# Kernel optimization log

Hardware: AMD Instinct MI355X
Metric: run time of the kernel (lower is better)

## Reference

```python
import jax, jax.numpy as jnp
import numpy as np

B, DIN, DOUT, NC = 8192, 4096, 4096, 64


def setup_inputs() -> dict:
    key = jax.random.key(0)
    k1, k2, k3, k4, k5 = jax.random.split(key, 5)
    x = jax.random.normal(k1, (B, DIN), dtype=jnp.float32)
    cluster = jax.random.uniform(k2, (B, NC), dtype=jnp.float32)
    weight = jax.random.uniform(k3, (DIN, DOUT), dtype=jnp.float32,
                                minval=-0.25, maxval=0.25)
    # torch init is ones; perturb slightly so the modulation is non-trivial
    style_L = 1.0 + 0.1 * jax.random.normal(k4, (NC, DIN), dtype=jnp.float32)
    style_R = 1.0 + 0.1 * jax.random.normal(k5, (NC, DOUT), dtype=jnp.float32)
    return {"x": x, "cluster": cluster, "weight": weight,
            "style_L": style_L, "style_R": style_R}


def reference(x, cluster, weight, style_L, style_R):
    # tmp_L: (B, din), tmp_R: (B, dout)
    tmp_L = cluster @ style_L
    tmp_R = cluster @ style_R
    # Algebraically identical to (weight * outer(tmp_L, tmp_R)) applied per
    # sample: out[b,o] = sum_i x[b,i]*tmpL[b,i]*W[i,o]*tmpR[b,o].
    # Factorized form avoids the (B, din, dout) intermediate.
    return ((x * tmp_L) @ weight) * tmp_R
```

## Files before the change

### kernel.cpp

```cpp
#include <hip/hip_runtime.h>
#include <cstdint>

#define BB   8192
#define DIN  4096
#define DOUT 4096
#define NCL  64

typedef __bf16 bf16;
typedef __attribute__((ext_vector_type(8))) __bf16 bf16x8;
typedef __attribute__((ext_vector_type(4))) float   f32x4;

#define GAS(p) (reinterpret_cast<uint32_t __attribute__((address_space(1)))*>(reinterpret_cast<uintptr_t>(p)))
#define LAS(p) (reinterpret_cast<uint32_t __attribute__((address_space(3)))*>(reinterpret_cast<uintptr_t>(p)))

#define WAITV(n)  asm volatile("s_waitcnt vmcnt(" #n ")" ::: "memory")
#define WAITL()   asm volatile("s_waitcnt lgkmcnt(0)" ::: "memory")
#define BARR()    __builtin_amdgcn_s_barrier()
#define SCHED0()  __builtin_amdgcn_sched_barrier(0)
#define MFMA(a, b, c) __builtin_amdgcn_mfma_f32_16x16x32_bf16((a), (b), (c), 0, 0, 0)

__global__ __launch_bounds__(256) void prologue_kernel(
    const float* __restrict__ x, const float* __restrict__ cl,
    const float* __restrict__ sL, bf16* __restrict__ Ap,
    bf16* __restrict__ clb)
{
    __shared__ uint4 lds_u4[2048];
    char* lds = (char*)lds_u4;
    const int t    = threadIdx.x;
    const int lane = t & 63;
    const int w    = t >> 6;
    const int wm   = w >> 1, wn = w & 1;
    const int r0   = blockIdx.x * 128;
    const int c0   = blockIdx.y * 128;

    #pragma unroll
    for (int i = 0; i < 4; i++) {
        int tk  = t + i * 256;
        int row = tk >> 3, ch = tk & 7;
        const float* src = cl + (size_t)(r0 + row) * NCL + ch * 8;
        float4 v0 = *(const float4*)src;
        float4 v1 = *(const float4*)(src + 4);
        bf16x8 pk;
        pk[0]=(bf16)v0.x; pk[1]=(bf16)v0.y; pk[2]=(bf16)v0.z; pk[3]=(bf16)v0.w;
        pk[4]=(bf16)v1.x; pk[5]=(bf16)v1.y; pk[6]=(bf16)v1.z; pk[7]=(bf16)v1.w;
        *(bf16x8*)(lds + row * 128 + ((ch ^ (row & 7)) << 4)) = pk;
        if (blockIdx.y == 0)
            *(bf16x8*)(clb + (size_t)(r0 + row) * NCL + ch * 8) = pk;
    }
    #pragma unroll
    for (int i = 0; i < 4; i++) {
        int tk = t + i * 256;
        int n  = tk & 127, c = tk >> 7;
        bf16x8 pl;
        #pragma unroll
        for (int j = 0; j < 8; j++)
            pl[j] = (bf16)sL[(size_t)(c * 8 + j) * DIN + c0 + n];
        *(bf16x8*)(lds + 16384 + n * 128 + ((c ^ (n & 7)) << 4)) = pl;
    }
    __syncthreads();

    f32x4 accL[4][4] = {};
    #pragma unroll
    for (int s = 0; s < 2; s++) {
        bf16x8 a[4], bl[4];
        #pragma unroll
        for (int m = 0; m < 4; m++) {
            int row = wm * 64 + m * 16 + (lane & 15);
            int ch  = s * 4 + (lane >> 4);
            a[m] = *(bf16x8*)(lds + row * 128 + ((ch ^ (row & 7)) << 4));
        }
        #pragma unroll
        for (int n = 0; n < 4; n++) {
            int row = wn * 64 + n * 16 + (lane & 15);
            int ch  = s * 4 + (lane >> 4);
            bl[n] = *(bf16x8*)(lds + 16384 + row * 128 + ((ch ^ (row & 7)) << 4));
        }
        #pragma unroll
        for (int m = 0; m < 4; m++)
            #pragma unroll
            for (int n = 0; n < 4; n++)
                accL[m][n] = MFMA(a[m], bl[n], accL[m][n]);
    }

    #pragma unroll
    for (int m = 0; m < 4; m++) {
        int rbase = r0 + wm * 64 + m * 16 + ((lane >> 4) << 2);
        #pragma unroll
        for (int n = 0; n < 4; n++) {
            int col = c0 + wn * 64 + n * 16 + (lane & 15);
            #pragma unroll
            for (int j = 0; j < 4; j++) {
                size_t idx = (size_t)(rbase + j) * DIN + col;
                Ap[idx] = (bf16)(x[idx] * accL[m][n][j]);
            }
        }
    }
}

__global__ __launch_bounds__(256) void transpose_kernel(
    const float* __restrict__ W, bf16* __restrict__ Wt)
{
    const int t  = threadIdx.x;
    const int n  = blockIdx.x * 256 + t;
    const int k0 = blockIdx.y * 32;
    bf16x8 v[4];
    #pragma unroll
    for (int q = 0; q < 4; q++)
        #pragma unroll
        for (int j = 0; j < 8; j++)
            v[q][j] = (bf16)W[(size_t)(k0 + q * 8 + j) * DOUT + n];
    bf16* dst = Wt + (size_t)n * DIN + k0;
    #pragma unroll
    for (int q = 0; q < 4; q++)
        *(bf16x8*)(dst + q * 8) = v[q];
}

__global__ __launch_bounds__(256) void srt_kernel(
    const float* __restrict__ sR, bf16* __restrict__ srt)
{
    const int o = blockIdx.x * 256 + threadIdx.x;
    bf16x8 v[8];
    #pragma unroll
    for (int q = 0; q < 8; q++)
        #pragma unroll
        for (int j = 0; j < 8; j++)
            v[q][j] = (bf16)sR[(size_t)(q * 8 + j) * DOUT + o];
    bf16* dst = srt + (size_t)o * 64;
    #pragma unroll
    for (int q = 0; q < 8; q++)
        *(bf16x8*)(dst + q * 8) = v[q];
}

template<int CUR>
__device__ __forceinline__ void tile_step(char* lds, int tid,
    const bf16* pA1, const bf16* pA2, const bf16* pA3, const bf16* pA4,
    const bf16* pB1, const bf16* pB2, const bf16* pB3, const bf16* pB4,
    int kA1, int kA2, int aoff0, int aoff1, int boff0, int boff1,
    bf16x8 a[4][2], bf16x8 b[4][2], f32x4 acc[8][4])
{
    constexpr int CB = CUR * 65536;
    constexpr int OB = (CUR ^ 1) * 65536;

    #pragma unroll
    for (int mq = 0; mq < 4; ++mq) {
        a[mq][0] = *(const bf16x8*)(lds + CB + mq * 2048 + aoff0);
        a[mq][1] = *(const bf16x8*)(lds + CB + mq * 2048 + aoff1);
    }
    #pragma unroll
    for (int nb = 0; nb < 4; ++nb) {
        b[nb][0] = *(const bf16x8*)(lds + CB + nb * 2048 + boff0);
        b[nb][1] = *(const bf16x8*)(lds + CB + nb * 2048 + boff1);
    }
    __builtin_amdgcn_global_load_lds(GAS(pA3 + kA1), LAS(lds + OB + 16384 + tid * 16), 16, 0, 0);
    __builtin_amdgcn_global_load_lds(GAS(pA4 + kA1), LAS(lds + OB + 24576 + tid * 16), 16, 0, 0);
    BARR();
    WAITL(); SCHED0();
    __builtin_amdgcn_s_setprio(1);
    #pragma unroll
    for (int k = 0; k < 2; ++k)
        #pragma unroll
        for (int mq = 0; mq < 4; ++mq)
            #pragma unroll
            for (int nq = 0; nq < 2; ++nq)
                acc[mq][nq] = MFMA(a[mq][k], b[nq][k], acc[mq][nq]);
    __builtin_amdgcn_s_setprio(0);
    BARR();

    __builtin_amdgcn_global_load_lds(GAS(pB1 + kA2), LAS(lds + CB + 32768 + tid * 16), 16, 0, 0);
    __builtin_amdgcn_global_load_lds(GAS(pB2 + kA2), LAS(lds + CB + 40960 + tid * 16), 16, 0, 0);
    BARR();
    __builtin_amdgcn_s_setprio(1);
    #pragma unroll
    for (int k = 0; k < 2; ++k)
        #pragma unroll
        for (int mq = 0; mq < 4; ++mq)
            #pragma unroll
            for (int nq = 0; nq < 2; ++nq)
                acc[mq][2 + nq] = MFMA(a[mq][k], b[2 + nq][k], acc[mq][2 + nq]);
    __builtin_amdgcn_s_setprio(0);
    BARR();

    #pragma unroll
    for (int mq = 0; mq < 4; ++mq) {
        a[mq][0] = *(const bf16x8*)(lds + CB + 8192 + mq * 2048 + aoff0);
        a[mq][1] = *(const bf16x8*)(lds + CB + 8192 + mq * 2048 + aoff1);
    }
    __builtin_amdgcn_global_load_lds(GAS(pB3 + kA2), LAS(lds + CB + 49152 + tid * 16), 16, 0, 0);
    __builtin_amdgcn_global_load_lds(GAS(pB4 + kA2), LAS(lds + CB + 57344 + tid * 16), 16, 0, 0);
    BARR();
    WAITL(); SCHED0();
    __builtin_amdgcn_s_setprio(1);
    #pragma unroll
    for (int k = 0; k < 2; ++k)
        #pragma unroll
        for (int mq = 0; mq < 4; ++mq)
            #pragma unroll
            for (int nq = 0; nq < 2; ++nq)
                acc[4 + mq][2 + nq] = MFMA(a[mq][k], b[2 + nq][k], acc[4 + mq][2 + nq]);
    __builtin_amdgcn_s_setprio(0);
    BARR();

    __builtin_amdgcn_global_load_lds(GAS(pA1 + kA2), LAS(lds + CB + tid * 16), 16, 0, 0);
    __builtin_amdgcn_global_load_lds(GAS(pA2 + kA2), LAS(lds + CB + 8192 + tid * 16), 16, 0, 0);
    BARR();
    __builtin_amdgcn_s_setprio(1);
    #pragma unroll
    for (int k = 0; k < 2; ++k)
        #pragma unroll
        for (int mq = 0; mq < 4; ++mq)
            #pragma unroll
            for (int nq = 0; nq < 2; ++nq)
                acc[4 + mq][nq] = MFMA(a[mq][k], b[nq][k], acc[4 + mq][nq]);
    __builtin_amdgcn_s_setprio(0);
    WAITV(6);
    BARR();
}

__global__ __launch_bounds__(512, 2) void gemm_kernel(
    const bf16* __restrict__ Ap, const bf16* __restrict__ Wt,
    const bf16* __restrict__ clb, const bf16* __restrict__ srt,
    float* __restrict__ out)
{
    __shared__ uint4 smem[8192];
    char* lds = (char*)smem;
    const int tid  = threadIdx.x;
    const int lane = tid & 63;
    const int w    = tid >> 6;
    const int wm   = w >> 2;
    const int wn   = w & 3;
    const int L = lane & 15, H = lane >> 4;

    const int bid = blockIdx.x;
    const int xc  = bid & 7, ii = bid >> 3;
    const int mt  = xc * 4 + (ii >> 4);
    const int nt  = ii & 15;
    const size_t brow = (size_t)mt * 256;
    const size_t bcol = (size_t)nt * 256;

    const int r1  = tid >> 3;
    const int gch = (tid & 7) ^ (r1 & 7);
    const bf16* pA1 = Ap + (brow + r1) * (size_t)DIN + gch * 8;
    const bf16* pA2 = pA1 + (size_t)64  * DIN;
    const bf16* pA3 = pA1 + (size_t)128 * DIN;
    const bf16* pA4 = pA1 + (size_t)192 * DIN;
    const bf16* pB1 = Wt + (bcol + r1) * (size_t)DIN + gch * 8;
    const bf16* pB2 = pB1 + (size_t)64  * DIN;
    const bf16* pB3 = pB1 + (size_t)128 * DIN;
    const bf16* pB4 = pB1 + (size_t)192 * DIN;

    const int swz0 = (H ^ (L & 7)) << 4;
    const int swz1 = ((4 + H) ^ (L & 7)) << 4;
    const int aoff0 = wm * 16384 + L * 128 + swz0;
    const int aoff1 = wm * 16384 + L * 128 + swz1;
    const int boff0 = 32768 + (wn >> 1) * 16384 + (wn & 1) * 8192 + L * 128 + swz0;
    const int boff1 = 32768 + (wn >> 1) * 16384 + (wn & 1) * 8192 + L * 128 + swz1;

    bf16x8 a[4][2], b[4][2];
    f32x4 acc[8][4] = {};

    __builtin_amdgcn_global_load_lds(GAS(pA1), LAS(lds + tid * 16), 16, 0, 0);
    __builtin_amdgcn_global_load_lds(GAS(pA2), LAS(lds + 8192 + tid * 16), 16, 0, 0);
    __builtin_amdgcn_global_load_lds(GAS(pA3), LAS(lds + 16384 + tid * 16), 16, 0, 0);
    __builtin_amdgcn_global_load_lds(GAS(pA4), LAS(lds + 24576 + tid * 16), 16, 0, 0);
    __builtin_amdgcn_global_load_lds(GAS(pB1), LAS(lds + 32768 + tid * 16), 16, 0, 0);
    __builtin_amdgcn_global_load_lds(GAS(pB2), LAS(lds + 40960 + tid * 16), 16, 0, 0);
    __builtin_amdgcn_global_load_lds(GAS(pB3), LAS(lds + 49152 + tid * 16), 16, 0, 0);
    __builtin_amdgcn_global_load_lds(GAS(pB4), LAS(lds + 57344 + tid * 16), 16, 0, 0);
    __builtin_amdgcn_global_load_lds(GAS(pB1 + 64), LAS(lds + 65536 + 32768 + tid * 16), 16, 0, 0);
    __builtin_amdgcn_global_load_lds(GAS(pB2 + 64), LAS(lds + 65536 + 40960 + tid * 16), 16, 0, 0);
    __builtin_amdgcn_global_load_lds(GAS(pB3 + 64), LAS(lds + 65536 + 49152 + tid * 16), 16, 0, 0);
    __builtin_amdgcn_global_load_lds(GAS(pB4 + 64), LAS(lds + 65536 + 57344 + tid * 16), 16, 0, 0);
    __builtin_amdgcn_global_load_lds(GAS(pA1 + 64), LAS(lds + 65536 + tid * 16), 16, 0, 0);
    __builtin_amdgcn_global_load_lds(GAS(pA2 + 64), LAS(lds + 65536 + 8192 + tid * 16), 16, 0, 0);
    WAITV(6);
    BARR();

    #pragma unroll 1
    for (int t = 0; t < 64; t += 2) {
        tile_step<0>(lds, tid, pA1, pA2, pA3, pA4, pB1, pB2, pB3, pB4,
                     ((t + 1) & 63) * 64, ((t + 2) & 63) * 64,
                     aoff0, aoff1, boff0, boff1, a, b, acc);
        tile_step<1>(lds, tid, pA1, pA2, pA3, pA4, pB1, pB2, pB3, pB4,
                     ((t + 2) & 63) * 64, ((t + 3) & 63) * 64,
                     aoff0, aoff1, boff0, boff1, a, b, acc);
    }

    WAITV(0);
    const bf16* pC = clb + (brow + r1) * 64 + gch * 8;
    const bf16* pR = srt + (bcol + r1) * 64 + gch * 8;
    __builtin_amdgcn_global_load_lds(GAS(pC),         LAS(lds + tid * 16), 16, 0, 0);
    __builtin_amdgcn_global_load_lds(GAS(pC + 4096),  LAS(lds + 8192 + tid * 16), 16, 0, 0);
    __builtin_amdgcn_global_load_lds(GAS(pC + 8192),  LAS(lds + 16384 + tid * 16), 16, 0, 0);
    __builtin_amdgcn_global_load_lds(GAS(pC + 12288), LAS(lds + 24576 + tid * 16), 16, 0, 0);
    __builtin_amdgcn_global_load_lds(GAS(pR),         LAS(lds + 32768 + tid * 16), 16, 0, 0);
    __builtin_amdgcn_global_load_lds(GAS(pR + 4096),  LAS(lds + 40960 + tid * 16), 16, 0, 0);
    __builtin_amdgcn_global_load_lds(GAS(pR + 8192),  LAS(lds + 49152 + tid * 16), 16, 0, 0);
    __builtin_amdgcn_global_load_lds(GAS(pR + 12288), LAS(lds + 57344 + tid * 16), 16, 0, 0);
    WAITV(0);
    BARR();

    #pragma unroll
    for (int nb = 0; nb < 4; ++nb) {
        b[nb][0] = *(const bf16x8*)(lds + nb * 2048 + boff0);
        b[nb][1] = *(const bf16x8*)(lds + nb * 2048 + boff1);
    }
    #pragma unroll
    for (int half = 0; half < 2; ++half) {
        #pragma unroll
        for (int mq = 0; mq < 4; ++mq) {
            a[mq][0] = *(const bf16x8*)(lds + half * 8192 + mq * 2048 + aoff0);
            a[mq][1] = *(const bf16x8*)(lds + half * 8192 + mq * 2048 + aoff1);
        }
        WAITL(); SCHED0();
        f32x4 r4[4][4] = {};
        #pragma unroll
        for (int k = 0; k < 2; ++k)
            #pragma unroll
            for (int mq = 0; mq < 4; ++mq)
                #pragma unroll
                for (int nb = 0; nb < 4; ++nb)
                    r4[mq][nb] = MFMA(a[mq][k], b[nb][k], r4[mq][nb]);
        #pragma unroll
        for (int mq = 0; mq < 4; ++mq)
            #pragma unroll
            for (int nb = 0; nb < 4; ++nb)
                acc[half * 4 + mq][nb] *= r4[mq][nb];
    }

    #pragma unroll
    for (int m = 0; m < 8; m++) {
        size_t rbase = brow + (size_t)(wm * 128 + m * 16 + (H << 2));
        #pragma unroll
        for (int n = 0; n < 4; n++) {
            size_t col = bcol + (size_t)(wn * 64 + n * 16 + L);
            #pragma unroll
            for (int j = 0; j < 4; j++) {
                size_t idx = (rbase + j) * DOUT + col;
                out[idx] = acc[m][n][j];
            }
        }
    }
}

extern "C" void kernel_launch(void* const* d_in, const int* in_sizes, int n_in,
                              void* d_out, int out_size, void* d_ws, size_t ws_size,
                              hipStream_t stream)
{
    (void)in_sizes; (void)n_in; (void)out_size;
    const float* x  = (const float*)d_in[0];
    const float* cl = (const float*)d_in[1];
    const float* W  = (const float*)d_in[2];
    const float* sL = (const float*)d_in[3];
    const float* sR = (const float*)d_in[4];
    float* out = (float*)d_out;

    const size_t AP_BYTES = (size_t)BB * DIN * sizeof(bf16);
    const size_t WT_BYTES = (size_t)DIN * DOUT * sizeof(bf16);
    const size_t CL_BYTES = (size_t)BB * NCL * sizeof(bf16);
    const size_t SR_BYTES = (size_t)DOUT * NCL * sizeof(bf16);
    if (ws_size < AP_BYTES + WT_BYTES + CL_BYTES + SR_BYTES) return;

    char* ws = (char*)d_ws;
    bf16* Ap  = (bf16*)ws;
    bf16* Wt  = (bf16*)(ws + AP_BYTES);
    bf16* clb = (bf16*)(ws + AP_BYTES + WT_BYTES);
    bf16* srt = (bf16*)(ws + AP_BYTES + WT_BYTES + CL_BYTES);

    prologue_kernel<<<dim3(BB / 128, DIN / 128), 256, 0, stream>>>(x, cl, sL, Ap, clb);
    transpose_kernel<<<dim3(DOUT / 256, DIN / 32), 256, 0, stream>>>(W, Wt);
    srt_kernel<<<dim3(DOUT / 256), 256, 0, stream>>>(sR, srt);
    gemm_kernel<<<dim3((BB / 256) * (DOUT / 256)), 512, 0, stream>>>(Ap, Wt, clb, srt, out);
}
```

Baseline: 330.6 us.

## Switch main GEMM to 32x32x16 MFMA with reworked per-warp tiling and load order

```diff
diff --git a/kernel.cpp b/kernel.cpp
--- a/kernel.cpp
+++ b/kernel.cpp
@@ -7,17 +7,20 @@
 #define NCL  64
 
 typedef __bf16 bf16;
-typedef __attribute__((ext_vector_type(8))) __bf16 bf16x8;
-typedef __attribute__((ext_vector_type(4))) float   f32x4;
+typedef __attribute__((ext_vector_type(8)))  __bf16 bf16x8;
+typedef __attribute__((ext_vector_type(4)))  float  f32x4;
+typedef __attribute__((ext_vector_type(16))) float  f32x16;
 
 #define GAS(p) (reinterpret_cast<uint32_t __attribute__((address_space(1)))*>(reinterpret_cast<uintptr_t>(p)))
 #define LAS(p) (reinterpret_cast<uint32_t __attribute__((address_space(3)))*>(reinterpret_cast<uintptr_t>(p)))
 
 #define WAITV(n)  asm volatile("s_waitcnt vmcnt(" #n ")" ::: "memory")
+#define WAITLN(n) asm volatile("s_waitcnt lgkmcnt(" #n ")" ::: "memory")
 #define WAITL()   asm volatile("s_waitcnt lgkmcnt(0)" ::: "memory")
 #define BARR()    __builtin_amdgcn_s_barrier()
 #define SCHED0()  __builtin_amdgcn_sched_barrier(0)
-#define MFMA(a, b, c) __builtin_amdgcn_mfma_f32_16x16x32_bf16((a), (b), (c), 0, 0, 0)
+#define MFMA16(a, b, c) __builtin_amdgcn_mfma_f32_16x16x32_bf16((a), (b), (c), 0, 0, 0)
+#define MFMA32(a, b, c) __builtin_amdgcn_mfma_f32_32x32x16_bf16((a), (b), (c), 0, 0, 0)
 
 __global__ __launch_bounds__(256) void prologue_kernel(
     const float* __restrict__ x, const float* __restrict__ cl,
@@ -79,7 +82,7 @@
         for (int m = 0; m < 4; m++)
             #pragma unroll
             for (int n = 0; n < 4; n++)
-                accL[m][n] = MFMA(a[m], bl[n], accL[m][n]);
+                accL[m][n] = MFMA16(a[m], bl[n], accL[m][n]);
     }
 
     #pragma unroll
@@ -135,82 +138,79 @@
 __device__ __forceinline__ void tile_step(char* lds, int tid,
     const bf16* pA1, const bf16* pA2, const bf16* pA3, const bf16* pA4,
     const bf16* pB1, const bf16* pB2, const bf16* pB3, const bf16* pB4,
-    int kA1, int kA2, int aoff0, int aoff1, int boff0, int boff1,
-    bf16x8 a[4][2], bf16x8 b[4][2], f32x4 acc[8][4])
+    int kA1, int kA2, int arow, int brow,
+    int ks0, int ks1, int ks2, int ks3,
+    bf16x8 (&a)[2][4], bf16x8 (&b0)[4], bf16x8 (&b1)[4], f32x16 (&acc)[4][2])
 {
     constexpr int CB = CUR * 65536;
     constexpr int OB = (CUR ^ 1) * 65536;
-
-    #pragma unroll
-    for (int mq = 0; mq < 4; ++mq) {
-        a[mq][0] = *(const bf16x8*)(lds + CB + mq * 2048 + aoff0);
-        a[mq][1] = *(const bf16x8*)(lds + CB + mq * 2048 + aoff1);
-    }
-    #pragma unroll
-    for (int nb = 0; nb < 4; ++nb) {
-        b[nb][0] = *(const bf16x8*)(lds + CB + nb * 2048 + boff0);
-        b[nb][1] = *(const bf16x8*)(lds + CB + nb * 2048 + boff1);
-    }
+    const int ks[4] = {ks0, ks1, ks2, ks3};
+
+    #pragma unroll
+    for (int f = 0; f < 2; ++f)
+        #pragma unroll
+        for (int kk = 0; kk < 4; ++kk)
+            a[f][kk] = *(const bf16x8*)(lds + CB + f * 4096 + arow + ks[kk]);
+    #pragma unroll
+    for (int kk = 0; kk < 4; ++kk)
+        b0[kk] = *(const bf16x8*)(lds + CB + 32768 + brow + ks[kk]);
     __builtin_amdgcn_global_load_lds(GAS(pA3 + kA1), LAS(lds + OB + 16384 + tid * 16), 16, 0, 0);
     __builtin_amdgcn_global_load_lds(GAS(pA4 + kA1), LAS(lds + OB + 24576 + tid * 16), 16, 0, 0);
+    WAITLN(8);
     BARR();
     WAITL(); SCHED0();
     __builtin_amdgcn_s_setprio(1);
     #pragma unroll
-    for (int k = 0; k < 2; ++k)
-        #pragma unroll
-        for (int mq = 0; mq < 4; ++mq)
-            #pragma unroll
-            for (int nq = 0; nq < 2; ++nq)
-                acc[mq][nq] = MFMA(a[mq][k], b[nq][k], acc[mq][nq]);
+    for (int kk = 0; kk < 4; ++kk)
+        #pragma unroll
+        for (int f = 0; f < 2; ++f)
+            acc[f][0] = MFMA32(a[f][kk], b0[kk], acc[f][0]);
     __builtin_amdgcn_s_setprio(0);
     BARR();
 
+    #pragma unroll
+    for (int kk = 0; kk < 4; ++kk)
+        b1[kk] = *(const bf16x8*)(lds + CB + 49152 + brow + ks[kk]);
+    __builtin_amdgcn_global_load_lds(GAS(pA1 + kA2), LAS(lds + CB + tid * 16), 16, 0, 0);
+    __builtin_amdgcn_global_load_lds(GAS(pA2 + kA2), LAS(lds + CB + 8192 + tid * 16), 16, 0, 0);
+    BARR();
+    WAITL(); SCHED0();
+    __builtin_amdgcn_s_setprio(1);
+    #pragma unroll
+    for (int kk = 0; kk < 4; ++kk)
+        #pragma unroll
+        for (int f = 0; f < 2; ++f)
+            acc[f][1] = MFMA32(a[f][kk], b1[kk], acc[f][1]);
+    __builtin_amdgcn_s_setprio(0);
+    BARR();
+
+    #pragma unroll
+    for (int f = 0; f < 2; ++f)
+        #pragma unroll
+        for (int kk = 0; kk < 4; ++kk)
+            a[f][kk] = *(const bf16x8*)(lds + CB + 16384 + f * 4096 + arow + ks[kk]);
     __builtin_amdgcn_global_load_lds(GAS(pB1 + kA2), LAS(lds + CB + 32768 + tid * 16), 16, 0, 0);
     __builtin_amdgcn_global_load_lds(GAS(pB2 + kA2), LAS(lds + CB + 40960 + tid * 16), 16, 0, 0);
     BARR();
+    WAITL(); SCHED0();
     __builtin_amdgcn_s_setprio(1);
     #pragma unroll
-    for (int k = 0; k < 2; ++k)
-        #pragma unroll
-        for (int mq = 0; mq < 4; ++mq)
-            #pragma unroll
-            for (int nq = 0; nq < 2; ++nq)
-                acc[mq][2 + nq] = MFMA(a[mq][k], b[2 + nq][k], acc[mq][2 + nq]);
+    for (int kk = 0; kk < 4; ++kk)
+        #pragma unroll
+        for (int f = 0; f < 2; ++f)
+            acc[2 + f][1] = MFMA32(a[f][kk], b1[kk], acc[2 + f][1]);
     __builtin_amdgcn_s_setprio(0);
     BARR();
 
-    #pragma unroll
-    for (int mq = 0; mq < 4; ++mq) {
-        a[mq][0] = *(const bf16x8*)(lds + CB + 8192 + mq * 2048 + aoff0);
-        a[mq][1] = *(const bf16x8*)(lds + CB + 8192 + mq * 2048 + aoff1);
-    }
     __builtin_amdgcn_global_load_lds(GAS(pB3 + kA2), LAS(lds + CB + 49152 + tid * 16), 16, 0, 0);
     __builtin_amdgcn_global_load_lds(GAS(pB4 + kA2), LAS(lds + CB + 57344 + tid * 16), 16, 0, 0);
     BARR();
-    WAITL(); SCHED0();
     __builtin_amdgcn_s_setprio(1);
     #pragma unroll
-    for (int k = 0; k < 2; ++k)
-        #pragma unroll
-        for (int mq = 0; mq < 4; ++mq)
-            #pragma unroll
-            for (int nq = 0; nq < 2; ++nq)
-                acc[4 + mq][2 + nq] = MFMA(a[mq][k], b[2 + nq][k], acc[4 + mq][2 + nq]);
-    __builtin_amdgcn_s_setprio(0);
-    BARR();
-
-    __builtin_amdgcn_global_load_lds(GAS(pA1 + kA2), LAS(lds + CB + tid * 16), 16, 0, 0);
-    __builtin_amdgcn_global_load_lds(GAS(pA2 + kA2), LAS(lds + CB + 8192 + tid * 16), 16, 0, 0);
-    BARR();
-    __builtin_amdgcn_s_setprio(1);
-    #pragma unroll
-    for (int k = 0; k < 2; ++k)
-        #pragma unroll
-        for (int mq = 0; mq < 4; ++mq)
-            #pragma unroll
-            for (int nq = 0; nq < 2; ++nq)
-                acc[4 + mq][nq] = MFMA(a[mq][k], b[nq][k], acc[4 + mq][nq]);
+    for (int kk = 0; kk < 4; ++kk)
+        #pragma unroll
+        for (int f = 0; f < 2; ++f)
+            acc[2 + f][0] = MFMA32(a[f][kk], b0[kk], acc[2 + f][0]);
     __builtin_amdgcn_s_setprio(0);
     WAITV(6);
     BARR();
@@ -228,35 +228,35 @@
     const int w    = tid >> 6;
     const int wm   = w >> 2;
     const int wn   = w & 3;
-    const int L = lane & 15, H = lane >> 4;
+    const int L5 = lane & 31, H1 = lane >> 5;
 
     const int bid = blockIdx.x;
     const int xc  = bid & 7, ii = bid >> 3;
     const int mt  = xc * 4 + (ii >> 4);
     const int nt  = ii & 15;
-    const size_t brow = (size_t)mt * 256;
-    const size_t bcol = (size_t)nt * 256;
+    const size_t brow_g = (size_t)mt * 256;
+    const size_t bcol_g = (size_t)nt * 256;
 
     const int r1  = tid >> 3;
     const int gch = (tid & 7) ^ (r1 & 7);
-    const bf16* pA1 = Ap + (brow + r1) * (size_t)DIN + gch * 8;
+    const bf16* pA1 = Ap + (brow_g + r1) * (size_t)DIN + gch * 8;
     const bf16* pA2 = pA1 + (size_t)64  * DIN;
     const bf16* pA3 = pA1 + (size_t)128 * DIN;
     const bf16* pA4 = pA1 + (size_t)192 * DIN;
-    const bf16* pB1 = Wt + (bcol + r1) * (size_t)DIN + gch * 8;
+    const bf16* pB1 = Wt + (bcol_g + r1) * (size_t)DIN + gch * 8;
     const bf16* pB2 = pB1 + (size_t)64  * DIN;
     const bf16* pB3 = pB1 + (size_t)128 * DIN;
     const bf16* pB4 = pB1 + (size_t)192 * DIN;
 
-    const int swz0 = (H ^ (L & 7)) << 4;
-    const int swz1 = ((4 + H) ^ (L & 7)) << 4;
-    const int aoff0 = wm * 16384 + L * 128 + swz0;
-    const int aoff1 = wm * 16384 + L * 128 + swz1;
-    const int boff0 = 32768 + (wn >> 1) * 16384 + (wn & 1) * 8192 + L * 128 + swz0;
-    const int boff1 = 32768 + (wn >> 1) * 16384 + (wn & 1) * 8192 + L * 128 + swz1;
-
-    bf16x8 a[4][2], b[4][2];
-    f32x4 acc[8][4] = {};
+    const int ks0 = (((0 * 2 + H1) ^ (L5 & 7)) << 4);
+    const int ks1 = (((1 * 2 + H1) ^ (L5 & 7)) << 4);
+    const int ks2 = (((2 * 2 + H1) ^ (L5 & 7)) << 4);
+    const int ks3 = (((3 * 2 + H1) ^ (L5 & 7)) << 4);
+    const int arow = (wm * 64 + L5) * 128;
+    const int brow = (wn * 32 + L5) * 128;
+
+    bf16x8 a[2][4], b0[4], b1[4];
+    f32x16 acc[4][2] = {};
 
     __builtin_amdgcn_global_load_lds(GAS(pA1), LAS(lds + tid * 16), 16, 0, 0);
     __builtin_amdgcn_global_load_lds(GAS(pA2), LAS(lds + 8192 + tid * 16), 16, 0, 0);
@@ -266,12 +266,12 @@
     __builtin_amdgcn_global_load_lds(GAS(pB2), LAS(lds + 40960 + tid * 16), 16, 0, 0);
     __builtin_amdgcn_global_load_lds(GAS(pB3), LAS(lds + 49152 + tid * 16), 16, 0, 0);
     __builtin_amdgcn_global_load_lds(GAS(pB4), LAS(lds + 57344 + tid * 16), 16, 0, 0);
+    __builtin_amdgcn_global_load_lds(GAS(pA1 + 64), LAS(lds + 65536 + tid * 16), 16, 0, 0);
+    __builtin_amdgcn_global_load_lds(GAS(pA2 + 64), LAS(lds + 65536 + 8192 + tid * 16), 16, 0, 0);
     __builtin_amdgcn_global_load_lds(GAS(pB1 + 64), LAS(lds + 65536 + 32768 + tid * 16), 16, 0, 0);
     __builtin_amdgcn_global_load_lds(GAS(pB2 + 64), LAS(lds + 65536 + 40960 + tid * 16), 16, 0, 0);
     __builtin_amdgcn_global_load_lds(GAS(pB3 + 64), LAS(lds + 65536 + 49152 + tid * 16), 16, 0, 0);
     __builtin_amdgcn_global_load_lds(GAS(pB4 + 64), LAS(lds + 65536 + 57344 + tid * 16), 16, 0, 0);
-    __builtin_amdgcn_global_load_lds(GAS(pA1 + 64), LAS(lds + 65536 + tid * 16), 16, 0, 0);
-    __builtin_amdgcn_global_load_lds(GAS(pA2 + 64), LAS(lds + 65536 + 8192 + tid * 16), 16, 0, 0);
     WAITV(6);
     BARR();
 
@@ -279,15 +279,15 @@
     for (int t = 0; t < 64; t += 2) {
         tile_step<0>(lds, tid, pA1, pA2, pA3, pA4, pB1, pB2, pB3, pB4,
                      ((t + 1) & 63) * 64, ((t + 2) & 63) * 64,
-                     aoff0, aoff1, boff0, boff1, a, b, acc);
+                     arow, brow, ks0, ks1, ks2, ks3, a, b0, b1, acc);
         tile_step<1>(lds, tid, pA1, pA2, pA3, pA4, pB1, pB2, pB3, pB4,
                      ((t + 2) & 63) * 64, ((t + 3) & 63) * 64,
-                     aoff0, aoff1, boff0, boff1, a, b, acc);
+                     arow, brow, ks0, ks1, ks2, ks3, a, b0, b1, acc);
     }
 
     WAITV(0);
-    const bf16* pC = clb + (brow + r1) * 64 + gch * 8;
-    const bf16* pR = srt + (bcol + r1) * 64 + gch * 8;
+    const bf16* pC = clb + (brow_g + r1) * 64 + gch * 8;
+    const bf16* pR = srt + (bcol_g + r1) * 64 + gch * 8;
     __builtin_amdgcn_global_load_lds(GAS(pC),         LAS(lds + tid * 16), 16, 0, 0);
     __builtin_amdgcn_global_load_lds(GAS(pC + 4096),  LAS(lds + 8192 + tid * 16), 16, 0, 0);
     __builtin_amdgcn_global_load_lds(GAS(pC + 8192),  LAS(lds + 16384 + tid * 16), 16, 0, 0);
@@ -299,44 +299,42 @@
     WAITV(0);
     BARR();
 
-    #pragma unroll
-    for (int nb = 0; nb < 4; ++nb) {
-        b[nb][0] = *(const bf16x8*)(lds + nb * 2048 + boff0);
-        b[nb][1] = *(const bf16x8*)(lds + nb * 2048 + boff1);
-    }
-    #pragma unroll
-    for (int half = 0; half < 2; ++half) {
-        #pragma unroll
-        for (int mq = 0; mq < 4; ++mq) {
-            a[mq][0] = *(const bf16x8*)(lds + half * 8192 + mq * 2048 + aoff0);
-            a[mq][1] = *(const bf16x8*)(lds + half * 8192 + mq * 2048 + aoff1);
-        }
+    const int ks[4] = {ks0, ks1, ks2, ks3};
+    bf16x8 cb[2][4];
+    #pragma unroll
+    for (int nf = 0; nf < 2; ++nf)
+        #pragma unroll
+        for (int kk = 0; kk < 4; ++kk)
+            cb[nf][kk] = *(const bf16x8*)(lds + 32768 + (nf * 2 + (wn >> 1)) * 8192
+                                          + ((wn & 1) * 32 + L5) * 128 + ks[kk]);
+    #pragma unroll
+    for (int mf = 0; mf < 4; ++mf) {
+        bf16x8 ca[4];
+        #pragma unroll
+        for (int kk = 0; kk < 4; ++kk)
+            ca[kk] = *(const bf16x8*)(lds + ((mf >> 1) * 2 + wm) * 8192
+                                      + ((mf & 1) * 32 + L5) * 128 + ks[kk]);
         WAITL(); SCHED0();
-        f32x4 r4[4][4] = {};
-        #pragma unroll
-        for (int k = 0; k < 2; ++k)
+        #pragma unroll
+        for (int nf = 0; nf < 2; ++nf) {
+            f32x16 r = {};
             #pragma unroll
-            for (int mq = 0; mq < 4; ++mq)
-                #pragma unroll
-                for (int nb = 0; nb < 4; ++nb)
-                    r4[mq][nb] = MFMA(a[mq][k], b[nb][k], r4[mq][nb]);
-        #pragma unroll
-        for (int mq = 0; mq < 4; ++mq)
+            for (int kk = 0; kk < 4; ++kk)
+                r = MFMA32(ca[kk], cb[nf][kk], r);
+            acc[mf][nf] *= r;
+        }
+    }
+
+    #pragma unroll
+    for (int mf = 0; mf < 4; ++mf) {
+        size_t rbase = brow_g + (size_t)((mf >> 1) * 128 + wm * 64 + (mf & 1) * 32 + 4 * H1);
+        #pragma unroll
+        for (int nf = 0; nf < 2; ++nf) {
+            size_t col = bcol_g + (size_t)(nf * 128 + wn * 32 + L5);
             #pragma unroll
-            for (int nb = 0; nb < 4; ++nb)
-                acc[half * 4 + mq][nb] *= r4[mq][nb];
-    }
-
-    #pragma unroll
-    for (int m = 0; m < 8; m++) {
-        size_t rbase = brow + (size_t)(wm * 128 + m * 16 + (H << 2));
-        #pragma unroll
-        for (int n = 0; n < 4; n++) {
-            size_t col = bcol + (size_t)(wn * 64 + n * 16 + L);
-            #pragma unroll
-            for (int j = 0; j < 4; j++) {
-                size_t idx = (rbase + j) * DOUT + col;
-                out[idx] = acc[m][n][j];
+            for (int reg = 0; reg < 16; ++reg) {
+                size_t row = rbase + (reg & 3) + 8 * (reg >> 2);
+                out[row * DOUT + col] = acc[mf][nf][reg];
             }
         }
     }
```

Measured after the change: 365.4 us. 10.5% more time.
